# Kernel optimization log

Measured on AMD Instinct MI355X. Metric: run time of the kernel, lower is better.

The kernel has to match this reference:

```python
import jax, jax.numpy as jnp
import numpy as np

B, S = 2, 2048
D_MODEL, N_HEAD = 2048, 16
D_K = D_MODEL // N_HEAD        # 128
D_C, D_CQ = 512, 1024
D_ROPE = 64
D_NOPE = D_K - D_ROPE          # 64
EPS = 1.1920929e-07            # torch.finfo(float32).eps (nn.RMSNorm default)


def rms_norm(x, w):
    var = jnp.mean(x * x, axis=-1, keepdims=True)
    return x * jax.lax.rsqrt(var + EPS) * w


def setup_inputs() -> dict:
    key = jax.random.key(0)
    ks = jax.random.split(key, 16)
    g = lambda k, shape: (jax.random.normal(k, shape, dtype=jnp.float32) * 0.02)
    return {
        "x": jax.random.normal(ks[0], (B, S, D_MODEL), dtype=jnp.float32),
        "q_down_w": g(ks[1], (D_CQ, D_MODEL)),
        "q_down_b": g(ks[2], (D_CQ,)),
        "q_norm_w": jnp.ones((D_CQ,), jnp.float32),
        "q_up_w": g(ks[3], (N_HEAD * D_K, D_CQ)),
        "q_up_b": g(ks[4], (N_HEAD * D_K,)),
        "kv_down_w": g(ks[5], (D_C, D_MODEL)),
        "kv_down_b": g(ks[6], (D_C,)),
        "kv_norm_w": jnp.ones((D_C,), jnp.float32),
        "kv_up_w": g(ks[7], (N_HEAD * (D_NOPE + D_K), D_C)),
        "kv_up_b": g(ks[8], (N_HEAD * (D_NOPE + D_K),)),
        "k_rope_w": g(ks[9], (N_HEAD * D_ROPE, D_MODEL)),
        "k_rope_b": g(ks[10], (N_HEAD * D_ROPE,)),
        "out_w": g(ks[11], (D_MODEL, D_MODEL)),
        "out_b": g(ks[12], (D_MODEL,)),
    }


def reference(x, q_down_w, q_down_b, q_norm_w, q_up_w, q_up_b,
              kv_down_w, kv_down_b, kv_norm_w, kv_up_w, kv_up_b,
              k_rope_w, k_rope_b, out_w, out_b):
    b, s, _ = x.shape
    # Q low-rank path: down -> RMSNorm -> up
    c_q = rms_norm(x @ q_down_w.T + q_down_b, q_norm_w)              # [b,s,d_cq]
    q = (c_q @ q_up_w.T + q_up_b).reshape(b, s, N_HEAD, D_K)
    q = jnp.transpose(q, (0, 2, 1, 3))                               # [b,h,s,d_k]
    q_nope, q_rope = q[..., :D_NOPE], q[..., D_NOPE:]
    # KV low-rank path
    c_kv = rms_norm(x @ kv_down_w.T + kv_down_b, kv_norm_w)          # [b,s,d_c]
    kv = (c_kv @ kv_up_w.T + kv_up_b).reshape(b, s, N_HEAD, D_NOPE + D_K)
    kv = jnp.transpose(kv, (0, 2, 1, 3))                             # [b,h,s,d_nope+d_k]
    k_nope, v = kv[..., :D_NOPE], kv[..., D_NOPE:]
    # decoupled rope subspace (rope=None config: no rotation applied)
    k_rope = (x @ k_rope_w.T + k_rope_b).reshape(b, s, N_HEAD, D_ROPE)
    k_rope = jnp.transpose(k_rope, (0, 2, 1, 3))                     # [b,h,s,d_rope]
    q = jnp.concatenate([q_nope, q_rope], axis=-1)                   # [b,h,s,d_k]
    k = jnp.concatenate([k_nope, k_rope], axis=-1)                   # [b,h,s,d_k]
    # causal attention
    scores = jnp.einsum('bhnd,bhmd->bhnm', q, k) / np.sqrt(D_K).astype(np.float32)
    mask = jnp.tril(jnp.ones((s, s), dtype=bool))
    scores = jnp.where(mask, scores, -jnp.inf)
    probs = jax.nn.softmax(scores, axis=-1)
    attn = jnp.einsum('bhnm,bhmd->bhnd', probs, v)                   # [b,h,s,d_k]
    attn = jnp.transpose(attn, (0, 2, 1, 3)).reshape(b, s, D_MODEL)
    return attn @ out_w.T + out_b
```

## Files before the change

kernel.cpp:

```cpp
#include <hip/hip_runtime.h>
#include <hip/hip_bf16.h>

typedef __attribute__((ext_vector_type(8))) short bf16x8;
typedef __attribute__((ext_vector_type(4))) float f32x4;
typedef unsigned short u16;

#define RMS_EPS 1.1920929e-07f

constexpr int Bb = 2, Ss = 2048, DM = 2048, NH = 16;
constexpr int MROWS = Bb * Ss;

__device__ __forceinline__ u16 f2bf(float f) {
    __hip_bfloat16 h = __float2bfloat16(f);
    return *reinterpret_cast<u16*>(&h);
}

__device__ __forceinline__ void gload16(const void* g, void* l) {
    __builtin_amdgcn_global_load_lds(
        (const __attribute__((address_space(1))) unsigned int*)g,
        (__attribute__((address_space(3))) unsigned int*)l, 16, 0, 0);
}

__global__ void cvt_f32_bf16(const float* __restrict__ in, u16* __restrict__ out, int n4) {
    int i = blockIdx.x * 256 + threadIdx.x;
    if (i >= n4) return;
    float4 v = reinterpret_cast<const float4*>(in)[i];
    ushort4 o;
    o.x = f2bf(v.x); o.y = f2bf(v.y); o.z = f2bf(v.z); o.w = f2bf(v.w);
    reinterpret_cast<ushort4*>(out)[i] = o;
}

__global__ void build_bcat(const float* __restrict__ qb, const float* __restrict__ kvb,
                           const float* __restrict__ krb, float* __restrict__ bcat) {
    int i = blockIdx.x * 256 + threadIdx.x;
    if (i < 1024) bcat[i] = qb[i];
    else if (i < 1536) bcat[i] = kvb[i - 1024];
    else if (i < 2560) bcat[i] = krb[i - 1536];
}

template <typename OutT>
__global__ __launch_bounds__(256) void gemm_bt(
    const u16* __restrict__ A, const u16* __restrict__ Bt,
    const float* __restrict__ bias, OutT* __restrict__ C,
    int M, int N, int K)
{
    __shared__ alignas(16) u16 sA[128 * 32];
    __shared__ alignas(16) u16 sB[128 * 32];
    const int tid = threadIdx.x;
    const int lane = tid & 63;
    const int w = tid >> 6;
    const int wr = w >> 1, wc = w & 1;
    const int l16 = lane & 15, lq = lane >> 4;
    const int tileM = blockIdx.y * 128;
    const int tileN = blockIdx.x * 128;

    f32x4 acc[4][4];
#pragma unroll
    for (int m = 0; m < 4; m++)
#pragma unroll
        for (int n = 0; n < 4; n++)
#pragma unroll
            for (int r = 0; r < 4; r++) acc[m][n][r] = 0.f;

    const int srow = w * 16 + (lane >> 2);
    const int scol = (lane & 3) * 8;
    const u16* gA0 = A + (size_t)(tileM + srow) * K + scol;
    const u16* gA1 = A + (size_t)(tileM + srow + 64) * K + scol;
    const u16* gB0 = Bt + (size_t)(tileN + srow) * K + scol;
    const u16* gB1 = Bt + (size_t)(tileN + srow + 64) * K + scol;
    u16* lA0 = sA + w * 512;
    u16* lA1 = sA + 2048 + w * 512;
    u16* lB0 = sB + w * 512;
    u16* lB1 = sB + 2048 + w * 512;

    int aoff[4], boff[4];
#pragma unroll
    for (int m = 0; m < 4; m++) aoff[m] = (wr * 64 + m * 16 + l16) * 32 + lq * 8;
#pragma unroll
    for (int n = 0; n < 4; n++) boff[n] = (wc * 64 + n * 16 + l16) * 32 + lq * 8;

    const int nk = K >> 5;
    for (int kk = 0; kk < nk; ++kk) {
        __syncthreads();
        gload16(gA0, lA0);
        gload16(gA1, lA1);
        gload16(gB0, lB0);
        gload16(gB1, lB1);
        gA0 += 32; gA1 += 32; gB0 += 32; gB1 += 32;
        __syncthreads();
        bf16x8 af[4], bfr[4];
#pragma unroll
        for (int m = 0; m < 4; m++) af[m] = *(const bf16x8*)&sA[aoff[m]];
#pragma unroll
        for (int n = 0; n < 4; n++) bfr[n] = *(const bf16x8*)&sB[boff[n]];
        __builtin_amdgcn_s_setprio(1);
#pragma unroll
        for (int m = 0; m < 4; m++)
#pragma unroll
            for (int n = 0; n < 4; n++)
                acc[m][n] = __builtin_amdgcn_mfma_f32_16x16x32_bf16(af[m], bfr[n], acc[m][n], 0, 0, 0);
        __builtin_amdgcn_s_setprio(0);
    }

#pragma unroll
    for (int n = 0; n < 4; n++) {
        int col = tileN + wc * 64 + n * 16 + l16;
        float bv = bias ? bias[col] : 0.f;
#pragma unroll
        for (int m = 0; m < 4; m++) {
            int rowb = tileM + wr * 64 + m * 16 + (lq << 2);
#pragma unroll
            for (int r = 0; r < 4; r++) {
                float v = acc[m][n][r] + bv;
                if constexpr (sizeof(OutT) == 2)
                    C[(size_t)(rowb + r) * N + col] = (OutT)f2bf(v);
                else
                    C[(size_t)(rowb + r) * N + col] = (OutT)v;
            }
        }
    }
}

__global__ __launch_bounds__(256) void gemm_down(
    const u16* __restrict__ A, const u16* __restrict__ Bt,
    const float* __restrict__ bcat, float* __restrict__ dcat,
    u16* __restrict__ krbuf)
{
    constexpr int K = 2048;
    __shared__ alignas(16) u16 sA[128 * 32];
    __shared__ alignas(16) u16 sB[128 * 32];
    const int tid = threadIdx.x;
    const int lane = tid & 63;
    const int w = tid >> 6;
    const int wr = w >> 1, wc = w & 1;
    const int l16 = lane & 15, lq = lane >> 4;
    const int tileM = blockIdx.y * 128;
    const int tileN = blockIdx.x * 128;

    f32x4 acc[4][4];
#pragma unroll
    for (int m = 0; m < 4; m++)
#pragma unroll
        for (int n = 0; n < 4; n++)
#pragma unroll
            for (int r = 0; r < 4; r++) acc[m][n][r] = 0.f;

    const int srow = w * 16 + (lane >> 2);
    const int scol = (lane & 3) * 8;
    const u16* gA0 = A + (size_t)(tileM + srow) * K + scol;
    const u16* gA1 = A + (size_t)(tileM + srow + 64) * K + scol;
    const u16* gB0 = Bt + (size_t)(tileN + srow) * K + scol;
    const u16* gB1 = Bt + (size_t)(tileN + srow + 64) * K + scol;
    u16* lA0 = sA + w * 512;
    u16* lA1 = sA + 2048 + w * 512;
    u16* lB0 = sB + w * 512;
    u16* lB1 = sB + 2048 + w * 512;

    int aoff[4], boff[4];
#pragma unroll
    for (int m = 0; m < 4; m++) aoff[m] = (wr * 64 + m * 16 + l16) * 32 + lq * 8;
#pragma unroll
    for (int n = 0; n < 4; n++) boff[n] = (wc * 64 + n * 16 + l16) * 32 + lq * 8;

    const int nk = K >> 5;
    for (int kk = 0; kk < nk; ++kk) {
        __syncthreads();
        gload16(gA0, lA0);
        gload16(gA1, lA1);
        gload16(gB0, lB0);
        gload16(gB1, lB1);
        gA0 += 32; gA1 += 32; gB0 += 32; gB1 += 32;
        __syncthreads();
        bf16x8 af[4], bfr[4];
#pragma unroll
        for (int m = 0; m < 4; m++) af[m] = *(const bf16x8*)&sA[aoff[m]];
#pragma unroll
        for (int n = 0; n < 4; n++) bfr[n] = *(const bf16x8*)&sB[boff[n]];
        __builtin_amdgcn_s_setprio(1);
#pragma unroll
        for (int m = 0; m < 4; m++)
#pragma unroll
            for (int n = 0; n < 4; n++)
                acc[m][n] = __builtin_amdgcn_mfma_f32_16x16x32_bf16(af[m], bfr[n], acc[m][n], 0, 0, 0);
        __builtin_amdgcn_s_setprio(0);
    }

    const bool isrope = (tileN >= 1536);
#pragma unroll
    for (int n = 0; n < 4; n++) {
        int col = tileN + wc * 64 + n * 16 + l16;
        float bv = bcat[col];
#pragma unroll
        for (int m = 0; m < 4; m++) {
            int rowb = tileM + wr * 64 + m * 16 + (lq << 2);
#pragma unroll
            for (int r = 0; r < 4; r++) {
                float v = acc[m][n][r] + bv;
                if (!isrope) dcat[(size_t)(rowb + r) * 1536 + col] = v;
                else         krbuf[(size_t)(rowb + r) * 1024 + (col - 1536)] = f2bf(v);
            }
        }
    }
}

template <int C>
__global__ __launch_bounds__(256) void rmsnorm_bf16(
    const float* __restrict__ in, int istride, const float* __restrict__ wgt, u16* __restrict__ out)
{
    const int row = blockIdx.x;
    const int tid = threadIdx.x;
    constexpr int PER = C / 256;
    const float* p = in + (size_t)row * istride;
    float v[PER];
    float ss = 0.f;
#pragma unroll
    for (int i = 0; i < PER; i++) { v[i] = p[tid + i * 256]; ss += v[i] * v[i]; }
#pragma unroll
    for (int o = 32; o; o >>= 1) ss += __shfl_xor(ss, o, 64);
    __shared__ float red[4];
    if ((tid & 63) == 0) red[tid >> 6] = ss;
    __syncthreads();
    float tot = red[0] + red[1] + red[2] + red[3];
    float inv = rsqrtf(tot / (float)C + RMS_EPS);
    u16* q = out + (size_t)row * C;
#pragma unroll
    for (int i = 0; i < PER; i++) {
        int c = tid + i * 256;
        q[c] = f2bf(v[i] * inv * wgt[c]);
    }
}

__global__ __launch_bounds__(256) void transpose_v(
    const u16* __restrict__ kvbuf, u16* __restrict__ vT)
{
    __shared__ alignas(16) u16 tile[64][72];
    const int tid = threadIdx.x;
    const int t0 = blockIdx.x * 64;
    const int h = blockIdx.y >> 1, dh = blockIdx.y & 1;
    const int trow = tid >> 2, c8 = (tid & 3) * 8;
    const u16* src = kvbuf + (size_t)(t0 + trow) * 3072 + h * 192 + 64 + dh * 64 + c8;
    *(bf16x8*)&tile[trow][c8]      = *(const bf16x8*)src;
    *(bf16x8*)&tile[trow][c8 + 32] = *(const bf16x8*)(src + 32);
    __syncthreads();
    const int drow = tid >> 2, tc8 = (tid & 3) * 8;
    bf16x8 a, b2;
#pragma unroll
    for (int j = 0; j < 8; j++) {
        a[j]  = (short)tile[tc8 + j][drow];
        b2[j] = (short)tile[tc8 + 32 + j][drow];
    }
    u16* dst = vT + (size_t)(h * 128 + dh * 64 + drow) * MROWS + t0 + tc8;
    *(bf16x8*)dst = a;
    *(bf16x8*)(dst + 32) = b2;
}

__global__ __launch_bounds__(256) void mla_attn(
    const u16* __restrict__ qbuf,
    const u16* __restrict__ kvbuf,
    const u16* __restrict__ krbuf,
    const u16* __restrict__ vT,
    u16* __restrict__ obuf)
{
    const int p = blockIdx.x;
    const int bh = blockIdx.y;
    const int b = bh >> 4, h = bh & 15;
    const int tid = threadIdx.x, lane = tid & 63, w = tid >> 6;
    const int l16 = lane & 15, lq = lane >> 4;

    __shared__ alignas(16) u16 sK[64 * 128];
    __shared__ alignas(16) u16 sVt[128 * 64];
    __shared__ alignas(16) u16 sPT[4][16 * 64];

    const int rowbase = b * Ss;
    char* pbase = (char*)sPT[w];

    const int sr = tid >> 2;
    const int sc = (tid & 3) * 32;
    const int vd = tid >> 1;
    const int vh = (tid & 1) * 32;
    const float scale = 0.08838834764831845f;

#pragma unroll
    for (int half = 0; half < 2; ++half) {
        const int qt = half ? (31 - p) : p;
        const int q0 = qt * 64;

        bf16x8 qf[4];
        {
            const u16* qp = qbuf + (size_t)(rowbase + q0 + w * 16 + l16) * 2048 + h * 128 + lq * 8;
#pragma unroll
            for (int c = 0; c < 4; c++) qf[c] = *(const bf16x8*)(qp + c * 32);
        }
        float mi = -1e30f, li = 0.f;
        f32x4 o[8];
#pragma unroll
        for (int d = 0; d < 8; d++)
#pragma unroll
            for (int r = 0; r < 4; r++) o[d][r] = 0.f;

        bf16x8 kr[4], vr[4];
        {
            const int krow = rowbase + sr;
            const u16* src = (sc < 64)
                ? kvbuf + (size_t)krow * 3072 + h * 192 + sc
                : krbuf + (size_t)krow * 1024 + h * 64 + (sc - 64);
#pragma unroll
            for (int j = 0; j < 4; j++) kr[j] = *(const bf16x8*)(src + j * 8);
            const u16* vsrc = vT + (size_t)(h * 128 + vd) * MROWS + rowbase + vh;
#pragma unroll
            for (int j = 0; j < 4; j++) vr[j] = *(const bf16x8*)(vsrc + j * 8);
        }

        for (int kt = 0; kt <= qt; ++kt) {
            __syncthreads();
#pragma unroll
            for (int j = 0; j < 4; j++) {
                int byteoff = sr * 256 + (sc + j * 8) * 2;
                *(bf16x8*)((char*)sK + (byteoff ^ ((sr & 7) << 4))) = kr[j];
            }
#pragma unroll
            for (int j = 0; j < 4; j++) {
                int byteoff = vd * 128 + (vh + j * 8) * 2;
                *(bf16x8*)((char*)sVt + (byteoff ^ ((vd & 7) << 4))) = vr[j];
            }
            __syncthreads();
            if (kt < qt) {
                const int krow = rowbase + (kt + 1) * 64 + sr;
                const u16* src = (sc < 64)
                    ? kvbuf + (size_t)krow * 3072 + h * 192 + sc
                    : krbuf + (size_t)krow * 1024 + h * 64 + (sc - 64);
#pragma unroll
                for (int j = 0; j < 4; j++) kr[j] = *(const bf16x8*)(src + j * 8);
                const u16* vsrc = vT + (size_t)(h * 128 + vd) * MROWS + rowbase + (kt + 1) * 64 + vh;
#pragma unroll
                for (int j = 0; j < 4; j++) vr[j] = *(const bf16x8*)(vsrc + j * 8);
            }

            f32x4 scf[4];
#pragma unroll
            for (int n = 0; n < 4; n++)
#pragma unroll
                for (int r = 0; r < 4; r++) scf[n][r] = 0.f;
            __builtin_amdgcn_s_setprio(1);
#pragma unroll
            for (int n = 0; n < 4; n++) {
#pragma unroll
                for (int c = 0; c < 4; c++) {
                    int row = n * 16 + l16;
                    int byteoff = row * 256 + (c * 32 + lq * 8) * 2;
                    bf16x8 kf = *(const bf16x8*)((char*)sK + (byteoff ^ ((row & 7) << 4)));
                    scf[n] = __builtin_amdgcn_mfma_f32_16x16x32_bf16(kf, qf[c], scf[n], 0, 0, 0);
                }
            }
            __builtin_amdgcn_s_setprio(0);

            const int qg = q0 + w * 16 + l16;
            float mnew = mi;
#pragma unroll
            for (int n = 0; n < 4; n++)
#pragma unroll
                for (int r = 0; r < 4; r++) {
                    int kg = kt * 64 + n * 16 + lq * 4 + r;
                    float s = scf[n][r] * scale;
                    s = (kg <= qg) ? s : -1e30f;
                    scf[n][r] = s;
                    mnew = fmaxf(mnew, s);
                }
            mnew = fmaxf(mnew, __shfl_xor(mnew, 16, 64));
            mnew = fmaxf(mnew, __shfl_xor(mnew, 32, 64));
            float rs = 0.f;
#pragma unroll
            for (int n = 0; n < 4; n++)
#pragma unroll
                for (int r = 0; r < 4; r++) {
                    float pv = __expf(scf[n][r] - mnew);
                    scf[n][r] = pv;
                    rs += pv;
                }
            rs += __shfl_xor(rs, 16, 64);
            rs += __shfl_xor(rs, 32, 64);
            float f = __expf(mi - mnew);
            li = li * f + rs;
            mi = mnew;
#pragma unroll
            for (int d = 0; d < 8; d++)
#pragma unroll
                for (int r = 0; r < 4; r++) o[d][r] *= f;

#pragma unroll
            for (int n = 0; n < 4; n++) {
                ushort4 pk;
                pk.x = f2bf(scf[n][0]); pk.y = f2bf(scf[n][1]);
                pk.z = f2bf(scf[n][2]); pk.w = f2bf(scf[n][3]);
                int byteoff = l16 * 128 + n * 32 + lq * 8;
                *(ushort4*)(pbase + (byteoff ^ ((l16 & 7) << 4))) = pk;
            }
            __builtin_amdgcn_s_setprio(1);
#pragma unroll
            for (int c = 0; c < 2; c++) {
                int pbyte = l16 * 128 + (c * 32 + lq * 8) * 2;
                bf16x8 pf = *(const bf16x8*)(pbase + (pbyte ^ ((l16 & 7) << 4)));
#pragma unroll
                for (int d = 0; d < 8; d++) {
                    int vrow = d * 16 + l16;
                    int vbyte = vrow * 128 + (c * 32 + lq * 8) * 2;
                    bf16x8 vf = *(const bf16x8*)((char*)sVt + (vbyte ^ ((vrow & 7) << 4)));
                    o[d] = __builtin_amdgcn_mfma_f32_16x16x32_bf16(vf, pf, o[d], 0, 0, 0);
                }
            }
            __builtin_amdgcn_s_setprio(0);
        }
        float invl = 1.f / li;
        u16* op = obuf + (size_t)(rowbase + q0 + w * 16 + l16) * 2048 + h * 128;
#pragma unroll
        for (int d = 0; d < 8; d++) {
            ushort4 ok;
            ok.x = f2bf(o[d][0] * invl); ok.y = f2bf(o[d][1] * invl);
            ok.z = f2bf(o[d][2] * invl); ok.w = f2bf(o[d][3] * invl);
            *(ushort4*)(op + d * 16 + lq * 4) = ok;
        }
    }
}

extern "C" void kernel_launch(void* const* d_in, const int* in_sizes, int n_in,
                              void* d_out, int out_size, void* d_ws, size_t ws_size,
                              hipStream_t stream) {
    const float* x        = (const float*)d_in[0];
    const float* q_down_w = (const float*)d_in[1];
    const float* q_down_b = (const float*)d_in[2];
    const float* q_norm_w = (const float*)d_in[3];
    const float* q_up_w   = (const float*)d_in[4];
    const float* q_up_b   = (const float*)d_in[5];
    const float* kv_down_w= (const float*)d_in[6];
    const float* kv_down_b= (const float*)d_in[7];
    const float* kv_norm_w= (const float*)d_in[8];
    const float* kv_up_w  = (const float*)d_in[9];
    const float* kv_up_b  = (const float*)d_in[10];
    const float* k_rope_w = (const float*)d_in[11];
    const float* k_rope_b = (const float*)d_in[12];
    const float* out_w    = (const float*)d_in[13];
    const float* out_b    = (const float*)d_in[14];

    char* ws = (char*)d_ws;
    u16* xbf    = (u16*)(ws + 0);
    u16* wcat   = (u16*)(ws + 16777216);
    u16* quw    = (u16*)(ws + 27262976);
    u16* kvuw   = (u16*)(ws + 31457280);
    u16* outw   = (u16*)(ws + 34603008);
    float* bcat = (float*)(ws + 42991616);
    float* dcat = (float*)(ws + 43008000);
    u16* cq     = (u16*)(ws + 68173824);
    u16* ckv    = (u16*)(ws + 76562432);
    u16* qbuf   = (u16*)(ws + 80756736);
    u16* kvbuf  = (u16*)(ws + 97533952);
    u16* krbuf  = (u16*)(ws + 122699776);
    u16* vT     = (u16*)(ws + 0);
    u16* attnbuf= (u16*)(ws + 43008000);

    auto cvt = [&](const float* src, u16* dst, int n) {
        int n4 = n / 4;
        cvt_f32_bf16<<<(n4 + 255) / 256, 256, 0, stream>>>(src, dst, n4);
    };
    cvt(x,         xbf,  MROWS * DM);
    cvt(q_down_w,  wcat,                1024 * 2048);
    cvt(kv_down_w, wcat + 1024 * 2048,  512 * 2048);
    cvt(k_rope_w,  wcat + 1536 * 2048,  1024 * 2048);
    cvt(q_up_w,    quw,  2048 * 1024);
    cvt(kv_up_w,   kvuw, 3072 * 512);
    cvt(out_w,     outw, 2048 * 2048);
    build_bcat<<<10, 256, 0, stream>>>(q_down_b, kv_down_b, k_rope_b, bcat);

    gemm_down<<<dim3(20, 32), 256, 0, stream>>>(xbf, wcat, bcat, dcat, krbuf);
    rmsnorm_bf16<1024><<<MROWS, 256, 0, stream>>>(dcat, 1536, q_norm_w, cq);
    rmsnorm_bf16<512><<<MROWS, 256, 0, stream>>>(dcat + 1024, 1536, kv_norm_w, ckv);
    gemm_bt<u16><<<dim3(16, 32), 256, 0, stream>>>(cq, quw, q_up_b, qbuf, MROWS, 2048, 1024);
    gemm_bt<u16><<<dim3(24, 32), 256, 0, stream>>>(ckv, kvuw, kv_up_b, kvbuf, MROWS, 3072, 512);
    transpose_v<<<dim3(64, 32), 256, 0, stream>>>(kvbuf, vT);
    mla_attn<<<dim3(16, Bb * NH), 256, 0, stream>>>(qbuf, kvbuf, krbuf, vT, attnbuf);
    gemm_bt<float><<<dim3(16, 32), 256, 0, stream>>>(attnbuf, outw, out_b, (float*)d_out, MROWS, 2048, 2048);
}
```

Measured before the change: 298.7 us.

## Enlarge attention Q tile to 128 rows, add lazy rescale, exp2 softmax, fused weight conversion

The attention kernel now processes 128 query rows per pass, with each wave handling two 16-row groups. Each K/V tile loaded into shared memory is therefore reused for twice as many queries, and the grid shrinks to 256 blocks. Blocks are remapped so heads group by XCD, fully masked tiles are skipped per wave, and masking is applied only on diagonal tiles. Softmax uses a raw v_exp_f32 with a folded log2e scale and rescales the accumulator only when the running max grows past a threshold. The seven f32-to-bf16 conversion launches are merged into one kernel. In exchange, register pressure is higher and there are fewer blocks to fill the device.

```diff
diff --git a/kernel.cpp b/kernel.cpp
--- a/kernel.cpp
+++ b/kernel.cpp
@@ -13,6 +13,10 @@
 __device__ __forceinline__ u16 f2bf(float f) {
     __hip_bfloat16 h = __float2bfloat16(f);
     return *reinterpret_cast<u16*>(&h);
+}
+
+__device__ __forceinline__ float exp2_fast(float x) {
+    float r; asm("v_exp_f32 %0, %1" : "=v"(r) : "v"(x)); return r;
 }
 
 __device__ __forceinline__ void gload16(const void* g, void* l) {
@@ -21,13 +25,29 @@
         (__attribute__((address_space(3))) unsigned int*)l, 16, 0, 0);
 }
 
-__global__ void cvt_f32_bf16(const float* __restrict__ in, u16* __restrict__ out, int n4) {
+__global__ __launch_bounds__(256) void cvt_all(
+    const float* __restrict__ s0, u16* __restrict__ d0,
+    const float* __restrict__ s1, u16* __restrict__ d1,
+    const float* __restrict__ s2, u16* __restrict__ d2,
+    const float* __restrict__ s3, u16* __restrict__ d3,
+    const float* __restrict__ s4, u16* __restrict__ d4,
+    const float* __restrict__ s5, u16* __restrict__ d5,
+    const float* __restrict__ s6, u16* __restrict__ d6)
+{
     int i = blockIdx.x * 256 + threadIdx.x;
-    if (i >= n4) return;
-    float4 v = reinterpret_cast<const float4*>(in)[i];
+    const float* s; u16* d; int off;
+    if (i < 2097152)      { s = s0; d = d0; off = 0; }
+    else if (i < 2621440) { s = s1; d = d1; off = 2097152; }
+    else if (i < 2883584) { s = s2; d = d2; off = 2621440; }
+    else if (i < 3407872) { s = s3; d = d3; off = 2883584; }
+    else if (i < 3932160) { s = s4; d = d4; off = 3407872; }
+    else if (i < 4325376) { s = s5; d = d5; off = 3932160; }
+    else                  { s = s6; d = d6; off = 4325376; }
+    int j = i - off;
+    float4 v = reinterpret_cast<const float4*>(s)[j];
     ushort4 o;
     o.x = f2bf(v.x); o.y = f2bf(v.y); o.z = f2bf(v.z); o.w = f2bf(v.w);
-    reinterpret_cast<ushort4*>(out)[i] = o;
+    reinterpret_cast<ushort4*>(d)[j] = o;
 }
 
 __global__ void build_bcat(const float* __restrict__ qb, const float* __restrict__ kvb,
@@ -261,42 +281,47 @@
     const u16* __restrict__ vT,
     u16* __restrict__ obuf)
 {
-    const int p = blockIdx.x;
-    const int bh = blockIdx.y;
+    const int flat = blockIdx.x + 8 * blockIdx.y;
+    const int xcd = flat & 7, ii = flat >> 3;
+    const int bh = xcd * 4 + (ii >> 3);
+    const int p  = ii & 7;
     const int b = bh >> 4, h = bh & 15;
     const int tid = threadIdx.x, lane = tid & 63, w = tid >> 6;
     const int l16 = lane & 15, lq = lane >> 4;
 
     __shared__ alignas(16) u16 sK[64 * 128];
     __shared__ alignas(16) u16 sVt[128 * 64];
-    __shared__ alignas(16) u16 sPT[4][16 * 64];
+    __shared__ alignas(16) u16 sP[8][16 * 64];
 
     const int rowbase = b * Ss;
-    char* pbase = (char*)sPT[w];
-
-    const int sr = tid >> 2;
-    const int sc = (tid & 3) * 32;
-    const int vd = tid >> 1;
-    const int vh = (tid & 1) * 32;
-    const float scale = 0.08838834764831845f;
-
-#pragma unroll
-    for (int half = 0; half < 2; ++half) {
-        const int qt = half ? (31 - p) : p;
-        const int q0 = qt * 64;
-
-        bf16x8 qf[4];
-        {
-            const u16* qp = qbuf + (size_t)(rowbase + q0 + w * 16 + l16) * 2048 + h * 128 + lq * 8;
-#pragma unroll
-            for (int c = 0; c < 4; c++) qf[c] = *(const bf16x8*)(qp + c * 32);
-        }
-        float mi = -1e30f, li = 0.f;
-        f32x4 o[8];
-#pragma unroll
-        for (int d = 0; d < 8; d++)
-#pragma unroll
-            for (int r = 0; r < 4; r++) o[d][r] = 0.f;
+    const int sr = tid >> 2, sc = (tid & 3) * 32;
+    const int vd = tid >> 1, vh = (tid & 1) * 32;
+    const float C1 = 0.12751742f;
+    const float THRR = 90.5f;
+
+#pragma unroll 1
+    for (int pass = 0; pass < 2; ++pass) {
+        const int qt = pass ? (15 - p) : p;
+        const int q0 = qt * 128;
+        const int nkt = 2 * qt + 2;
+
+        bf16x8 qf[2][4];
+#pragma unroll
+        for (int g = 0; g < 2; ++g) {
+            const u16* qp = qbuf + (size_t)(rowbase + q0 + w * 32 + g * 16 + l16) * 2048 + h * 128 + lq * 8;
+#pragma unroll
+            for (int c = 0; c < 4; c++) qf[g][c] = *(const bf16x8*)(qp + c * 32);
+        }
+        float mi[2], li[2];
+        f32x4 o[2][8];
+#pragma unroll
+        for (int g = 0; g < 2; ++g) {
+            mi[g] = -3e38f; li[g] = 0.f;
+#pragma unroll
+            for (int d = 0; d < 8; d++)
+#pragma unroll
+                for (int r = 0; r < 4; r++) o[g][d][r] = 0.f;
+        }
 
         bf16x8 kr[4], vr[4];
         {
@@ -311,7 +336,7 @@
             for (int j = 0; j < 4; j++) vr[j] = *(const bf16x8*)(vsrc + j * 8);
         }
 
-        for (int kt = 0; kt <= qt; ++kt) {
+        for (int kt = 0; kt < nkt; ++kt) {
             __syncthreads();
 #pragma unroll
             for (int j = 0; j < 4; j++) {
@@ -324,7 +349,7 @@
                 *(bf16x8*)((char*)sVt + (byteoff ^ ((vd & 7) << 4))) = vr[j];
             }
             __syncthreads();
-            if (kt < qt) {
+            if (kt + 1 < nkt) {
                 const int krow = rowbase + (kt + 1) * 64 + sr;
                 const u16* src = (sc < 64)
                     ? kvbuf + (size_t)krow * 3072 + h * 192 + sc
@@ -336,88 +361,115 @@
                 for (int j = 0; j < 4; j++) vr[j] = *(const bf16x8*)(vsrc + j * 8);
             }
 
-            f32x4 scf[4];
-#pragma unroll
-            for (int n = 0; n < 4; n++)
-#pragma unroll
-                for (int r = 0; r < 4; r++) scf[n][r] = 0.f;
-            __builtin_amdgcn_s_setprio(1);
-#pragma unroll
-            for (int n = 0; n < 4; n++) {
-#pragma unroll
-                for (int c = 0; c < 4; c++) {
-                    int row = n * 16 + l16;
-                    int byteoff = row * 256 + (c * 32 + lq * 8) * 2;
-                    bf16x8 kf = *(const bf16x8*)((char*)sK + (byteoff ^ ((row & 7) << 4)));
-                    scf[n] = __builtin_amdgcn_mfma_f32_16x16x32_bf16(kf, qf[c], scf[n], 0, 0, 0);
+            const bool alive = (kt * 64) <= (q0 + w * 32 + 15);
+            if (alive) {
+                f32x4 scf[2][4];
+#pragma unroll
+                for (int g = 0; g < 2; ++g)
+#pragma unroll
+                    for (int n = 0; n < 4; n++)
+#pragma unroll
+                        for (int r = 0; r < 4; r++) scf[g][n][r] = 0.f;
+                __builtin_amdgcn_s_setprio(1);
+#pragma unroll
+                for (int n = 0; n < 4; n++) {
+#pragma unroll
+                    for (int c = 0; c < 4; c++) {
+                        int row = n * 16 + l16;
+                        int byteoff = row * 256 + (c * 32 + lq * 8) * 2;
+                        bf16x8 kf = *(const bf16x8*)((char*)sK + (byteoff ^ ((row & 7) << 4)));
+                        scf[0][n] = __builtin_amdgcn_mfma_f32_16x16x32_bf16(kf, qf[0][c], scf[0][n], 0, 0, 0);
+                        scf[1][n] = __builtin_amdgcn_mfma_f32_16x16x32_bf16(kf, qf[1][c], scf[1][n], 0, 0, 0);
+                    }
                 }
-            }
-            __builtin_amdgcn_s_setprio(0);
-
-            const int qg = q0 + w * 16 + l16;
-            float mnew = mi;
-#pragma unroll
-            for (int n = 0; n < 4; n++)
-#pragma unroll
-                for (int r = 0; r < 4; r++) {
-                    int kg = kt * 64 + n * 16 + lq * 4 + r;
-                    float s = scf[n][r] * scale;
-                    s = (kg <= qg) ? s : -1e30f;
-                    scf[n][r] = s;
-                    mnew = fmaxf(mnew, s);
+                __builtin_amdgcn_s_setprio(0);
+
+#pragma unroll
+                for (int g = 0; g < 2; ++g) {
+                    const int base = q0 + w * 32 + g * 16;
+                    if (kt * 64 + 63 > base) {
+                        const int qg = base + l16;
+#pragma unroll
+                        for (int n = 0; n < 4; n++)
+#pragma unroll
+                            for (int r = 0; r < 4; r++) {
+                                int kg = kt * 64 + n * 16 + lq * 4 + r;
+                                if (kg > qg) scf[g][n][r] = -3e38f;
+                            }
+                    }
+                    float mx = mi[g];
+#pragma unroll
+                    for (int n = 0; n < 4; n++)
+#pragma unroll
+                        for (int r = 0; r < 4; r++) mx = fmaxf(mx, scf[g][n][r]);
+                    mx = fmaxf(mx, __shfl_xor(mx, 16, 64));
+                    mx = fmaxf(mx, __shfl_xor(mx, 32, 64));
+                    if (!__all(mx - mi[g] <= THRR)) {
+                        float f = exp2_fast((mi[g] - mx) * C1);
+                        li[g] *= f;
+#pragma unroll
+                        for (int d = 0; d < 8; d++)
+#pragma unroll
+                            for (int r = 0; r < 4; r++) o[g][d][r] *= f;
+                        mi[g] = mx;
+                    }
+                    float mc = mi[g] * C1;
+                    float rs = 0.f;
+#pragma unroll
+                    for (int n = 0; n < 4; n++)
+#pragma unroll
+                        for (int r = 0; r < 4; r++) {
+                            float pv = exp2_fast(__fmaf_rn(scf[g][n][r], C1, -mc));
+                            scf[g][n][r] = pv;
+                            rs += pv;
+                        }
+                    rs += __shfl_xor(rs, 16, 64);
+                    rs += __shfl_xor(rs, 32, 64);
+                    li[g] += rs;
+                    char* pb = (char*)sP + ((w << 1) | g) * 2048;
+#pragma unroll
+                    for (int n = 0; n < 4; n++) {
+                        ushort4 pk;
+                        pk.x = f2bf(scf[g][n][0]); pk.y = f2bf(scf[g][n][1]);
+                        pk.z = f2bf(scf[g][n][2]); pk.w = f2bf(scf[g][n][3]);
+                        int byteoff = l16 * 128 + n * 32 + lq * 8;
+                        *(ushort4*)(pb + (byteoff ^ ((l16 & 7) << 4))) = pk;
+                    }
                 }
-            mnew = fmaxf(mnew, __shfl_xor(mnew, 16, 64));
-            mnew = fmaxf(mnew, __shfl_xor(mnew, 32, 64));
-            float rs = 0.f;
-#pragma unroll
-            for (int n = 0; n < 4; n++)
-#pragma unroll
-                for (int r = 0; r < 4; r++) {
-                    float pv = __expf(scf[n][r] - mnew);
-                    scf[n][r] = pv;
-                    rs += pv;
+
+                __builtin_amdgcn_s_setprio(1);
+#pragma unroll
+                for (int c = 0; c < 2; c++) {
+                    bf16x8 pf[2];
+#pragma unroll
+                    for (int g = 0; g < 2; ++g) {
+                        char* pb = (char*)sP + ((w << 1) | g) * 2048;
+                        int pbyte = l16 * 128 + (c * 32 + lq * 8) * 2;
+                        pf[g] = *(const bf16x8*)(pb + (pbyte ^ ((l16 & 7) << 4)));
+                    }
+#pragma unroll
+                    for (int d = 0; d < 8; d++) {
+                        int vrow = d * 16 + l16;
+                        int vbyte = vrow * 128 + (c * 32 + lq * 8) * 2;
+                        bf16x8 vf = *(const bf16x8*)((char*)sVt + (vbyte ^ ((vrow & 7) << 4)));
+                        o[0][d] = __builtin_amdgcn_mfma_f32_16x16x32_bf16(vf, pf[0], o[0][d], 0, 0, 0);
+                        o[1][d] = __builtin_amdgcn_mfma_f32_16x16x32_bf16(vf, pf[1], o[1][d], 0, 0, 0);
+                    }
                 }
-            rs += __shfl_xor(rs, 16, 64);
-            rs += __shfl_xor(rs, 32, 64);
-            float f = __expf(mi - mnew);
-            li = li * f + rs;
-            mi = mnew;
-#pragma unroll
-            for (int d = 0; d < 8; d++)
-#pragma unroll
-                for (int r = 0; r < 4; r++) o[d][r] *= f;
-
-#pragma unroll
-            for (int n = 0; n < 4; n++) {
-                ushort4 pk;
-                pk.x = f2bf(scf[n][0]); pk.y = f2bf(scf[n][1]);
-                pk.z = f2bf(scf[n][2]); pk.w = f2bf(scf[n][3]);
-                int byteoff = l16 * 128 + n * 32 + lq * 8;
-                *(ushort4*)(pbase + (byteoff ^ ((l16 & 7) << 4))) = pk;
-            }
-            __builtin_amdgcn_s_setprio(1);
-#pragma unroll
-            for (int c = 0; c < 2; c++) {
-                int pbyte = l16 * 128 + (c * 32 + lq * 8) * 2;
-                bf16x8 pf = *(const bf16x8*)(pbase + (pbyte ^ ((l16 & 7) << 4)));
-#pragma unroll
-                for (int d = 0; d < 8; d++) {
-                    int vrow = d * 16 + l16;
-                    int vbyte = vrow * 128 + (c * 32 + lq * 8) * 2;
-                    bf16x8 vf = *(const bf16x8*)((char*)sVt + (vbyte ^ ((vrow & 7) << 4)));
-                    o[d] = __builtin_amdgcn_mfma_f32_16x16x32_bf16(vf, pf, o[d], 0, 0, 0);
-                }
-            }
-            __builtin_amdgcn_s_setprio(0);
-        }
-        float invl = 1.f / li;
-        u16* op = obuf + (size_t)(rowbase + q0 + w * 16 + l16) * 2048 + h * 128;
-#pragma unroll
-        for (int d = 0; d < 8; d++) {
-            ushort4 ok;
-            ok.x = f2bf(o[d][0] * invl); ok.y = f2bf(o[d][1] * invl);
-            ok.z = f2bf(o[d][2] * invl); ok.w = f2bf(o[d][3] * invl);
-            *(ushort4*)(op + d * 16 + lq * 4) = ok;
+                __builtin_amdgcn_s_setprio(0);
+            }
+        }
+#pragma unroll
+        for (int g = 0; g < 2; ++g) {
+            float invl = 1.f / li[g];
+            u16* op = obuf + (size_t)(rowbase + q0 + w * 32 + g * 16 + l16) * 2048 + h * 128;
+#pragma unroll
+            for (int d = 0; d < 8; d++) {
+                ushort4 ok;
+                ok.x = f2bf(o[g][d][0] * invl); ok.y = f2bf(o[g][d][1] * invl);
+                ok.z = f2bf(o[g][d][2] * invl); ok.w = f2bf(o[g][d][3] * invl);
+                *(ushort4*)(op + d * 16 + lq * 4) = ok;
+            }
         }
     }
 }
@@ -457,17 +509,14 @@
     u16* vT     = (u16*)(ws + 0);
     u16* attnbuf= (u16*)(ws + 43008000);
 
-    auto cvt = [&](const float* src, u16* dst, int n) {
-        int n4 = n / 4;
-        cvt_f32_bf16<<<(n4 + 255) / 256, 256, 0, stream>>>(src, dst, n4);
-    };
-    cvt(x,         xbf,  MROWS * DM);
-    cvt(q_down_w,  wcat,                1024 * 2048);
-    cvt(kv_down_w, wcat + 1024 * 2048,  512 * 2048);
-    cvt(k_rope_w,  wcat + 1536 * 2048,  1024 * 2048);
-    cvt(q_up_w,    quw,  2048 * 1024);
-    cvt(kv_up_w,   kvuw, 3072 * 512);
-    cvt(out_w,     outw, 2048 * 2048);
+    cvt_all<<<20992, 256, 0, stream>>>(
+        x, xbf,
+        q_down_w,  wcat,
+        kv_down_w, wcat + 1024 * 2048,
+        k_rope_w,  wcat + 1536 * 2048,
+        q_up_w,    quw,
+        kv_up_w,   kvuw,
+        out_w,     outw);
     build_bcat<<<10, 256, 0, stream>>>(q_down_b, kv_down_b, k_rope_b, bcat);
 
     gemm_down<<<dim3(20, 32), 256, 0, stream>>>(xbf, wcat, bcat, dcat, krbuf);
@@ -476,6 +525,6 @@
     gemm_bt<u16><<<dim3(16, 32), 256, 0, stream>>>(cq, quw, q_up_b, qbuf, MROWS, 2048, 1024);
     gemm_bt<u16><<<dim3(24, 32), 256, 0, stream>>>(ckv, kvuw, kv_up_b, kvbuf, MROWS, 3072, 512);
     transpose_v<<<dim3(64, 32), 256, 0, stream>>>(kvbuf, vT);
-    mla_attn<<<dim3(16, Bb * NH), 256, 0, stream>>>(qbuf, kvbuf, krbuf, vT, attnbuf);
+    mla_attn<<<dim3(8, 32), 256, 0, stream>>>(qbuf, kvbuf, krbuf, vT, attnbuf);
     gemm_bt<float><<<dim3(16, 32), 256, 0, stream>>>(attnbuf, outw, out_b, (float*)d_out, MROWS, 2048, 2048);
 }
```

After: 285.4 us. 1.05x faster.

## Fuse bf16 conversions into one launch and restructure attention grid and softmax

Applied to the files above, without the earlier changes.

Merges the seven fp32-to-bf16 conversion launches into a single kernel that picks its source and destination by index range. The attention kernel goes from one block handling two paired query tiles to one block per query tile, with a reordered grid that interleaves heavy and light causal tiles. Softmax now uses native exp2 with a folded log2e-times-scale constant and applies the causal mask only on the diagonal tile. It also skips rescaling the running max unless the max grows past a threshold. These cut launch overhead and ALU work in the softmax, but change scheduling balance and make accuracy depend on the lazy-rescale threshold staying in range.

```diff
diff --git a/kernel.cpp b/kernel.cpp
--- a/kernel.cpp
+++ b/kernel.cpp
@@ -13,6 +13,10 @@
 __device__ __forceinline__ u16 f2bf(float f) {
     __hip_bfloat16 h = __float2bfloat16(f);
     return *reinterpret_cast<u16*>(&h);
+}
+
+__device__ __forceinline__ float exp2_fast(float x) {
+    float r; asm("v_exp_f32 %0, %1" : "=v"(r) : "v"(x)); return r;
 }
 
 __device__ __forceinline__ void gload16(const void* g, void* l) {
@@ -21,13 +25,29 @@
         (__attribute__((address_space(3))) unsigned int*)l, 16, 0, 0);
 }
 
-__global__ void cvt_f32_bf16(const float* __restrict__ in, u16* __restrict__ out, int n4) {
+__global__ __launch_bounds__(256) void cvt_all(
+    const float* __restrict__ s0, u16* __restrict__ d0,
+    const float* __restrict__ s1, u16* __restrict__ d1,
+    const float* __restrict__ s2, u16* __restrict__ d2,
+    const float* __restrict__ s3, u16* __restrict__ d3,
+    const float* __restrict__ s4, u16* __restrict__ d4,
+    const float* __restrict__ s5, u16* __restrict__ d5,
+    const float* __restrict__ s6, u16* __restrict__ d6)
+{
     int i = blockIdx.x * 256 + threadIdx.x;
-    if (i >= n4) return;
-    float4 v = reinterpret_cast<const float4*>(in)[i];
+    const float* s; u16* d; int off;
+    if (i < 2097152)      { s = s0; d = d0; off = 0; }
+    else if (i < 2621440) { s = s1; d = d1; off = 2097152; }
+    else if (i < 2883584) { s = s2; d = d2; off = 2621440; }
+    else if (i < 3407872) { s = s3; d = d3; off = 2883584; }
+    else if (i < 3932160) { s = s4; d = d4; off = 3407872; }
+    else if (i < 4325376) { s = s5; d = d5; off = 3932160; }
+    else                  { s = s6; d = d6; off = 4325376; }
+    int j = i - off;
+    float4 v = reinterpret_cast<const float4*>(s)[j];
     ushort4 o;
     o.x = f2bf(v.x); o.y = f2bf(v.y); o.z = f2bf(v.z); o.w = f2bf(v.w);
-    reinterpret_cast<ushort4*>(out)[i] = o;
+    reinterpret_cast<ushort4*>(d)[j] = o;
 }
 
 __global__ void build_bcat(const float* __restrict__ qb, const float* __restrict__ kvb,
@@ -261,8 +281,11 @@
     const u16* __restrict__ vT,
     u16* __restrict__ obuf)
 {
-    const int p = blockIdx.x;
-    const int bh = blockIdx.y;
+    const int bh = blockIdx.x;
+    const int yy = blockIdx.y;
+    const int ii = yy & 7, jj = yy >> 3;
+    const int qt = (jj == 0) ? (ii * 2) : (jj == 1) ? (31 - ii * 2)
+                 : (jj == 2) ? (ii * 2 + 1) : (30 - ii * 2);
     const int b = bh >> 4, h = bh & 15;
     const int tid = threadIdx.x, lane = tid & 63, w = tid >> 6;
     const int l16 = lane & 15, lq = lane >> 4;
@@ -272,153 +295,154 @@
     __shared__ alignas(16) u16 sPT[4][16 * 64];
 
     const int rowbase = b * Ss;
+    const int q0 = qt * 64;
     char* pbase = (char*)sPT[w];
 
-    const int sr = tid >> 2;
-    const int sc = (tid & 3) * 32;
-    const int vd = tid >> 1;
-    const int vh = (tid & 1) * 32;
-    const float scale = 0.08838834764831845f;
-
-#pragma unroll
-    for (int half = 0; half < 2; ++half) {
-        const int qt = half ? (31 - p) : p;
-        const int q0 = qt * 64;
-
-        bf16x8 qf[4];
-        {
-            const u16* qp = qbuf + (size_t)(rowbase + q0 + w * 16 + l16) * 2048 + h * 128 + lq * 8;
-#pragma unroll
-            for (int c = 0; c < 4; c++) qf[c] = *(const bf16x8*)(qp + c * 32);
-        }
-        float mi = -1e30f, li = 0.f;
-        f32x4 o[8];
-#pragma unroll
-        for (int d = 0; d < 8; d++)
-#pragma unroll
-            for (int r = 0; r < 4; r++) o[d][r] = 0.f;
-
-        bf16x8 kr[4], vr[4];
-        {
-            const int krow = rowbase + sr;
+    const int sr = tid >> 2, sc = (tid & 3) * 32;
+    const int vd = tid >> 1, vh = (tid & 1) * 32;
+    const float C1 = 0.12751742f;
+    const float THRR = 90.5f;
+
+    bf16x8 qf[4];
+    {
+        const u16* qp = qbuf + (size_t)(rowbase + q0 + w * 16 + l16) * 2048 + h * 128 + lq * 8;
+#pragma unroll
+        for (int c = 0; c < 4; c++) qf[c] = *(const bf16x8*)(qp + c * 32);
+    }
+    float mi = -3e38f, li = 0.f;
+    f32x4 o[8];
+#pragma unroll
+    for (int d = 0; d < 8; d++)
+#pragma unroll
+        for (int r = 0; r < 4; r++) o[d][r] = 0.f;
+
+    bf16x8 kr[4], vr[4];
+    {
+        const int krow = rowbase + sr;
+        const u16* src = (sc < 64)
+            ? kvbuf + (size_t)krow * 3072 + h * 192 + sc
+            : krbuf + (size_t)krow * 1024 + h * 64 + (sc - 64);
+#pragma unroll
+        for (int j = 0; j < 4; j++) kr[j] = *(const bf16x8*)(src + j * 8);
+        const u16* vsrc = vT + (size_t)(h * 128 + vd) * MROWS + rowbase + vh;
+#pragma unroll
+        for (int j = 0; j < 4; j++) vr[j] = *(const bf16x8*)(vsrc + j * 8);
+    }
+
+    for (int kt = 0; kt <= qt; ++kt) {
+        __syncthreads();
+#pragma unroll
+        for (int j = 0; j < 4; j++) {
+            int byteoff = sr * 256 + (sc + j * 8) * 2;
+            *(bf16x8*)((char*)sK + (byteoff ^ ((sr & 7) << 4))) = kr[j];
+        }
+#pragma unroll
+        for (int j = 0; j < 4; j++) {
+            int byteoff = vd * 128 + (vh + j * 8) * 2;
+            *(bf16x8*)((char*)sVt + (byteoff ^ ((vd & 7) << 4))) = vr[j];
+        }
+        __syncthreads();
+        if (kt < qt) {
+            const int krow = rowbase + (kt + 1) * 64 + sr;
             const u16* src = (sc < 64)
                 ? kvbuf + (size_t)krow * 3072 + h * 192 + sc
                 : krbuf + (size_t)krow * 1024 + h * 64 + (sc - 64);
 #pragma unroll
             for (int j = 0; j < 4; j++) kr[j] = *(const bf16x8*)(src + j * 8);
-            const u16* vsrc = vT + (size_t)(h * 128 + vd) * MROWS + rowbase + vh;
+            const u16* vsrc = vT + (size_t)(h * 128 + vd) * MROWS + rowbase + (kt + 1) * 64 + vh;
 #pragma unroll
             for (int j = 0; j < 4; j++) vr[j] = *(const bf16x8*)(vsrc + j * 8);
         }
 
-        for (int kt = 0; kt <= qt; ++kt) {
-            __syncthreads();
-#pragma unroll
-            for (int j = 0; j < 4; j++) {
-                int byteoff = sr * 256 + (sc + j * 8) * 2;
-                *(bf16x8*)((char*)sK + (byteoff ^ ((sr & 7) << 4))) = kr[j];
+        f32x4 scf[4];
+#pragma unroll
+        for (int n = 0; n < 4; n++)
+#pragma unroll
+            for (int r = 0; r < 4; r++) scf[n][r] = 0.f;
+        __builtin_amdgcn_s_setprio(1);
+#pragma unroll
+        for (int n = 0; n < 4; n++) {
+#pragma unroll
+            for (int c = 0; c < 4; c++) {
+                int row = n * 16 + l16;
+                int byteoff = row * 256 + (c * 32 + lq * 8) * 2;
+                bf16x8 kf = *(const bf16x8*)((char*)sK + (byteoff ^ ((row & 7) << 4)));
+                scf[n] = __builtin_amdgcn_mfma_f32_16x16x32_bf16(kf, qf[c], scf[n], 0, 0, 0);
             }
-#pragma unroll
-            for (int j = 0; j < 4; j++) {
-                int byteoff = vd * 128 + (vh + j * 8) * 2;
-                *(bf16x8*)((char*)sVt + (byteoff ^ ((vd & 7) << 4))) = vr[j];
+        }
+        __builtin_amdgcn_s_setprio(0);
+
+        if (kt == qt) {
+            const int qg = w * 16 + l16;
+#pragma unroll
+            for (int n = 0; n < 4; n++)
+#pragma unroll
+                for (int r = 0; r < 4; r++) {
+                    int kg = n * 16 + lq * 4 + r;
+                    if (kg > qg) scf[n][r] = -3e38f;
+                }
+        }
+        float mx = mi;
+#pragma unroll
+        for (int n = 0; n < 4; n++)
+#pragma unroll
+            for (int r = 0; r < 4; r++) mx = fmaxf(mx, scf[n][r]);
+        mx = fmaxf(mx, __shfl_xor(mx, 16, 64));
+        mx = fmaxf(mx, __shfl_xor(mx, 32, 64));
+        if (!__all(mx - mi <= THRR)) {
+            float f = exp2_fast((mi - mx) * C1);
+            li *= f;
+#pragma unroll
+            for (int d = 0; d < 8; d++)
+#pragma unroll
+                for (int r = 0; r < 4; r++) o[d][r] *= f;
+            mi = mx;
+        }
+        float mc = mi * C1;
+        float rs = 0.f;
+#pragma unroll
+        for (int n = 0; n < 4; n++)
+#pragma unroll
+            for (int r = 0; r < 4; r++) {
+                float pv = exp2_fast(__fmaf_rn(scf[n][r], C1, -mc));
+                scf[n][r] = pv;
+                rs += pv;
             }
-            __syncthreads();
-            if (kt < qt) {
-                const int krow = rowbase + (kt + 1) * 64 + sr;
-                const u16* src = (sc < 64)
-                    ? kvbuf + (size_t)krow * 3072 + h * 192 + sc
-                    : krbuf + (size_t)krow * 1024 + h * 64 + (sc - 64);
-#pragma unroll
-                for (int j = 0; j < 4; j++) kr[j] = *(const bf16x8*)(src + j * 8);
-                const u16* vsrc = vT + (size_t)(h * 128 + vd) * MROWS + rowbase + (kt + 1) * 64 + vh;
-#pragma unroll
-                for (int j = 0; j < 4; j++) vr[j] = *(const bf16x8*)(vsrc + j * 8);
+        rs += __shfl_xor(rs, 16, 64);
+        rs += __shfl_xor(rs, 32, 64);
+        li += rs;
+
+#pragma unroll
+        for (int n = 0; n < 4; n++) {
+            ushort4 pk;
+            pk.x = f2bf(scf[n][0]); pk.y = f2bf(scf[n][1]);
+            pk.z = f2bf(scf[n][2]); pk.w = f2bf(scf[n][3]);
+            int byteoff = l16 * 128 + n * 32 + lq * 8;
+            *(ushort4*)(pbase + (byteoff ^ ((l16 & 7) << 4))) = pk;
+        }
+        __builtin_amdgcn_s_setprio(1);
+#pragma unroll
+        for (int c = 0; c < 2; c++) {
+            int pbyte = l16 * 128 + (c * 32 + lq * 8) * 2;
+            bf16x8 pf = *(const bf16x8*)(pbase + (pbyte ^ ((l16 & 7) << 4)));
+#pragma unroll
+            for (int d = 0; d < 8; d++) {
+                int vrow = d * 16 + l16;
+                int vbyte = vrow * 128 + (c * 32 + lq * 8) * 2;
+                bf16x8 vf = *(const bf16x8*)((char*)sVt + (vbyte ^ ((vrow & 7) << 4)));
+                o[d] = __builtin_amdgcn_mfma_f32_16x16x32_bf16(vf, pf, o[d], 0, 0, 0);
             }
-
-            f32x4 scf[4];
-#pragma unroll
-            for (int n = 0; n < 4; n++)
-#pragma unroll
-                for (int r = 0; r < 4; r++) scf[n][r] = 0.f;
-            __builtin_amdgcn_s_setprio(1);
-#pragma unroll
-            for (int n = 0; n < 4; n++) {
-#pragma unroll
-                for (int c = 0; c < 4; c++) {
-                    int row = n * 16 + l16;
-                    int byteoff = row * 256 + (c * 32 + lq * 8) * 2;
-                    bf16x8 kf = *(const bf16x8*)((char*)sK + (byteoff ^ ((row & 7) << 4)));
-                    scf[n] = __builtin_amdgcn_mfma_f32_16x16x32_bf16(kf, qf[c], scf[n], 0, 0, 0);
-                }
-            }
-            __builtin_amdgcn_s_setprio(0);
-
-            const int qg = q0 + w * 16 + l16;
-            float mnew = mi;
-#pragma unroll
-            for (int n = 0; n < 4; n++)
-#pragma unroll
-                for (int r = 0; r < 4; r++) {
-                    int kg = kt * 64 + n * 16 + lq * 4 + r;
-                    float s = scf[n][r] * scale;
-                    s = (kg <= qg) ? s : -1e30f;
-                    scf[n][r] = s;
-                    mnew = fmaxf(mnew, s);
-                }
-            mnew = fmaxf(mnew, __shfl_xor(mnew, 16, 64));
-            mnew = fmaxf(mnew, __shfl_xor(mnew, 32, 64));
-            float rs = 0.f;
-#pragma unroll
-            for (int n = 0; n < 4; n++)
-#pragma unroll
-                for (int r = 0; r < 4; r++) {
-                    float pv = __expf(scf[n][r] - mnew);
-                    scf[n][r] = pv;
-                    rs += pv;
-                }
-            rs += __shfl_xor(rs, 16, 64);
-            rs += __shfl_xor(rs, 32, 64);
-            float f = __expf(mi - mnew);
-            li = li * f + rs;
-            mi = mnew;
-#pragma unroll
-            for (int d = 0; d < 8; d++)
-#pragma unroll
-                for (int r = 0; r < 4; r++) o[d][r] *= f;
-
-#pragma unroll
-            for (int n = 0; n < 4; n++) {
-                ushort4 pk;
-                pk.x = f2bf(scf[n][0]); pk.y = f2bf(scf[n][1]);
-                pk.z = f2bf(scf[n][2]); pk.w = f2bf(scf[n][3]);
-                int byteoff = l16 * 128 + n * 32 + lq * 8;
-                *(ushort4*)(pbase + (byteoff ^ ((l16 & 7) << 4))) = pk;
-            }
-            __builtin_amdgcn_s_setprio(1);
-#pragma unroll
-            for (int c = 0; c < 2; c++) {
-                int pbyte = l16 * 128 + (c * 32 + lq * 8) * 2;
-                bf16x8 pf = *(const bf16x8*)(pbase + (pbyte ^ ((l16 & 7) << 4)));
-#pragma unroll
-                for (int d = 0; d < 8; d++) {
-                    int vrow = d * 16 + l16;
-                    int vbyte = vrow * 128 + (c * 32 + lq * 8) * 2;
-                    bf16x8 vf = *(const bf16x8*)((char*)sVt + (vbyte ^ ((vrow & 7) << 4)));
-                    o[d] = __builtin_amdgcn_mfma_f32_16x16x32_bf16(vf, pf, o[d], 0, 0, 0);
-                }
-            }
-            __builtin_amdgcn_s_setprio(0);
-        }
-        float invl = 1.f / li;
-        u16* op = obuf + (size_t)(rowbase + q0 + w * 16 + l16) * 2048 + h * 128;
-#pragma unroll
-        for (int d = 0; d < 8; d++) {
-            ushort4 ok;
-            ok.x = f2bf(o[d][0] * invl); ok.y = f2bf(o[d][1] * invl);
-            ok.z = f2bf(o[d][2] * invl); ok.w = f2bf(o[d][3] * invl);
-            *(ushort4*)(op + d * 16 + lq * 4) = ok;
-        }
+        }
+        __builtin_amdgcn_s_setprio(0);
+    }
+    float invl = 1.f / li;
+    u16* op = obuf + (size_t)(rowbase + q0 + w * 16 + l16) * 2048 + h * 128;
+#pragma unroll
+    for (int d = 0; d < 8; d++) {
+        ushort4 ok;
+        ok.x = f2bf(o[d][0] * invl); ok.y = f2bf(o[d][1] * invl);
+        ok.z = f2bf(o[d][2] * invl); ok.w = f2bf(o[d][3] * invl);
+        *(ushort4*)(op + d * 16 + lq * 4) = ok;
     }
 }
 
@@ -457,17 +481,14 @@
     u16* vT     = (u16*)(ws + 0);
     u16* attnbuf= (u16*)(ws + 43008000);
 
-    auto cvt = [&](const float* src, u16* dst, int n) {
-        int n4 = n / 4;
-        cvt_f32_bf16<<<(n4 + 255) / 256, 256, 0, stream>>>(src, dst, n4);
-    };
-    cvt(x,         xbf,  MROWS * DM);
-    cvt(q_down_w,  wcat,                1024 * 2048);
-    cvt(kv_down_w, wcat + 1024 * 2048,  512 * 2048);
-    cvt(k_rope_w,  wcat + 1536 * 2048,  1024 * 2048);
-    cvt(q_up_w,    quw,  2048 * 1024);
-    cvt(kv_up_w,   kvuw, 3072 * 512);
-    cvt(out_w,     outw, 2048 * 2048);
+    cvt_all<<<20992, 256, 0, stream>>>(
+        x, xbf,
+        q_down_w,  wcat,
+        kv_down_w, wcat + 1024 * 2048,
+        k_rope_w,  wcat + 1536 * 2048,
+        q_up_w,    quw,
+        kv_up_w,   kvuw,
+        out_w,     outw);
     build_bcat<<<10, 256, 0, stream>>>(q_down_b, kv_down_b, k_rope_b, bcat);
 
     gemm_down<<<dim3(20, 32), 256, 0, stream>>>(xbf, wcat, bcat, dcat, krbuf);
@@ -476,6 +497,6 @@
     gemm_bt<u16><<<dim3(16, 32), 256, 0, stream>>>(cq, quw, q_up_b, qbuf, MROWS, 2048, 1024);
     gemm_bt<u16><<<dim3(24, 32), 256, 0, stream>>>(ckv, kvuw, kv_up_b, kvbuf, MROWS, 3072, 512);
     transpose_v<<<dim3(64, 32), 256, 0, stream>>>(kvbuf, vT);
-    mla_attn<<<dim3(16, Bb * NH), 256, 0, stream>>>(qbuf, kvbuf, krbuf, vT, attnbuf);
+    mla_attn<<<dim3(32, 32), 256, 0, stream>>>(qbuf, kvbuf, krbuf, vT, attnbuf);
     gemm_bt<float><<<dim3(16, 32), 256, 0, stream>>>(attnbuf, outw, out_b, (float*)d_out, MROWS, 2048, 2048);
 }
```

New measurement: 285.4 us. 4.5% less time.
